# Optimization experiments

Measured on AMD Instinct MI355X. Metric: run time of the kernel, lower is better.

Reference implementation:

```python
import jax, jax.numpy as jnp
import numpy as np

ANCHOR_SIZES = [64.0, 128.0, 256.0]
ANCHOR_RATIOS = [0.5, 1.0, 2.0]
STD_SCALING = 1.0
RPN_STRIDE = 16
PRE_NMS_TOP_N = 3000
POST_NMS_TOP_N = 300
NMS_IOU_THRES = 0.7


def make_anchors():
    # ratios are sqrt'd as in the original __init__; anchors stored as (w, h)
    rs = [np.sqrt(r) for r in ANCHOR_RATIOS]
    a = [[s * r, s / r] for s in ANCHOR_SIZES for r in rs]
    return np.array(a, dtype=np.float32)  # [A, 2]


def setup_inputs() -> dict:
    key = jax.random.key(0)
    k1, k2 = jax.random.split(key)
    B, A, H, W = 4, 9, 34, 60
    rpn_scores = jax.random.uniform(k1, (B, A, H, W), dtype=jnp.float32)
    rpn_deltas = jax.random.normal(k2, (B, 4 * A, H, W), dtype=jnp.float32)
    input_image = jnp.zeros((B, 3, 544, 960), dtype=jnp.float32)  # only shape is used
    return {"rpn_scores": rpn_scores, "rpn_deltas": rpn_deltas, "input_image": input_image}


def _pairwise_iou(boxes):
    # boxes: [N, 4] in (x1, y1, x2, y2)
    x1, y1, x2, y2 = boxes[:, 0], boxes[:, 1], boxes[:, 2], boxes[:, 3]
    area = (x2 - x1) * (y2 - y1)
    iw = jnp.maximum(jnp.minimum(x2[:, None], x2[None, :]) - jnp.maximum(x1[:, None], x1[None, :]), 0.0)
    ih = jnp.maximum(jnp.minimum(y2[:, None], y2[None, :]) - jnp.maximum(y1[:, None], y1[None, :]), 0.0)
    inter = iw * ih
    union = area[:, None] + area[None, :] - inter
    return inter / jnp.maximum(union, 1e-8)


def _nms_single(boxes, probs):
    # pre-NMS top-N by score, then greedy IoU suppression, then post-NMS top-N (zero-padded)
    scores_k, idx = jax.lax.top_k(probs, PRE_NMS_TOP_N)
    boxes_k = boxes[idx]                                 # [pre_N, 4]
    iou = _pairwise_iou(boxes_k)                         # [pre_N, pre_N]

    def body(active, i):
        keep_i = active[i]
        sup = (iou[i] > NMS_IOU_THRES) & keep_i
        sup = sup.at[i].set(False)
        return active & ~sup, keep_i

    _, keep = jax.lax.scan(body, jnp.ones((PRE_NMS_TOP_N,), bool), jnp.arange(PRE_NMS_TOP_N))
    sel = jnp.where(keep, scores_k, -jnp.inf)
    _, kidx = jax.lax.top_k(sel, POST_NMS_TOP_N)
    valid = keep[kidx]
    return jnp.where(valid[:, None], boxes_k[kidx], 0.0)  # [post_N, 4]


def _forward(rpn_scores, rpn_deltas, input_image):
    B, A, H, W = rpn_scores.shape
    img_h = jnp.float32(input_image.shape[2])
    img_w = jnp.float32(input_image.shape[3])
    # NCHW -> NHWC -> [B,H,W,A,4]; channel layout is anchor-major, coord-minor
    deltas = (rpn_deltas * (1.0 / STD_SCALING)).transpose(0, 2, 3, 1).reshape(B, H, W, A, 4)
    ancs = jnp.asarray(make_anchors())                   # [A, 2] (w, h)
    aw, ah = ancs[:, 0], ancs[:, 1]
    # anchor centers on the RPN grid, at input-image scale
    cx = jnp.broadcast_to(((jnp.arange(W, dtype=jnp.float32) + 0.5) * RPN_STRIDE)[None, :, None], (H, W, A))
    cy = jnp.broadcast_to(((jnp.arange(H, dtype=jnp.float32) + 0.5) * RPN_STRIDE)[:, None, None], (H, W, A))
    tx, ty, tw, th = deltas[..., 0], deltas[..., 1], deltas[..., 2], deltas[..., 3]
    ctr_x = cx + tx * aw
    ctr_y = cy + ty * ah
    w1 = jnp.exp(tw) * aw
    h1 = jnp.exp(th) * ah
    x1 = ctr_x - 0.5 * w1
    y1 = ctr_y - 0.5 * h1
    x2 = x1 + w1
    y2 = y1 + h1
    x1 = jnp.clip(x1, 0.0, img_w - 1.0)
    x2 = jnp.clip(x2, 0.0, img_w - 1.0)
    y1 = jnp.clip(y1, 0.0, img_h - 1.0)
    y2 = jnp.clip(y2, 0.0, img_h - 1.0)
    boxes = jnp.stack([x1, y1, x2, y2], axis=-1)          # [B,H,W,A,4]
    boxes = boxes.transpose(0, 3, 1, 2, 4).reshape(B, -1, 4)  # [B, A*H*W, 4] (matches score layout)
    probs = rpn_scores.reshape(B, -1)
    return jax.vmap(_nms_single)(boxes, probs)            # [B, post_N, 4]


def reference(rpn_scores, rpn_deltas, input_image):
    return _forward(rpn_scores, rpn_deltas, input_image)
```

## Files before the change

### kernel.cpp

```cpp
#include <hip/hip_runtime.h>
#include <stdint.h>

typedef uint32_t u32;
typedef uint64_t u64;

#define NB 4
#define NA 9
#define NH 34
#define NW 60
#define HW (NH*NW)
#define NBOX (NA*HW)
#define PRE_NMS 3000
#define POST_NMS 300
#define NBUCKET 4096
#define SEGCAP 4096
#define NTH 1024
#define PER 18
#define NCAND 1088
#define MWc 17
#define NCHK 17

__device__ __constant__ float c_aw[9] = {
  45.254833995939045f, 64.0f,  90.50966799187808f,
  90.50966799187808f,  128.0f, 181.01933598375617f,
  181.01933598375617f, 256.0f, 362.03867196751233f };
__device__ __constant__ float c_ah[9] = {
  90.50966799187808f,  64.0f,  45.254833995939045f,
  181.01933598375617f, 128.0f, 90.50966799187808f,
  362.03867196751233f, 256.0f, 181.01933598375617f };

__device__ __forceinline__ u64 readlane64(u64 v, int lane) {
  u32 lo = __builtin_amdgcn_readlane((u32)(v & 0xffffffffull), lane);
  u32 hi = __builtin_amdgcn_readlane((u32)(v >> 32), lane);
  return ((u64)hi << 32) | lo;
}

__device__ __forceinline__ float4 decode_box(const float* __restrict__ dl, int idx) {
  int a = idx / HW;
  int r = idx - a * HW;
  int h = r / NW;
  int w = r - h * NW;
  const float* dp = dl + (4 * a) * HW + r;
  float tx = dp[0];
  float ty = dp[HW];
  float tw = dp[2 * HW];
  float th = dp[3 * HW];
  float aw = c_aw[a], ah = c_ah[a];
  float ctr_x = ((float)w + 0.5f) * 16.0f + tx * aw;
  float ctr_y = ((float)h + 0.5f) * 16.0f + ty * ah;
  float w1 = expf(tw) * aw;
  float h1 = expf(th) * ah;
  float x1 = ctr_x - 0.5f * w1;
  float y1 = ctr_y - 0.5f * h1;
  float x2 = x1 + w1;
  float y2 = y1 + h1;
  x1 = fminf(fmaxf(x1, 0.0f), 959.0f);
  x2 = fminf(fmaxf(x2, 0.0f), 959.0f);
  y1 = fminf(fmaxf(y1, 0.0f), 543.0f);
  y2 = fminf(fmaxf(y2, 0.0f), 543.0f);
  return make_float4(x1, y1, x2, y2);
}

__global__ void __launch_bounds__(NTH)
topk_rank_decode_kernel(const float* __restrict__ scores,
                        const float* __restrict__ deltas,
                        float4* __restrict__ boxes_ws)
{
  __shared__ u32 s_base[NBUCKET];
  __shared__ u32 s_cnt[NBUCKET];
  __shared__ u64 s_keys[SEGCAP];
  __shared__ u32 s_sfx[NTH];

  const int tid = threadIdx.x;
  const int b   = blockIdx.x;
  const float* sc = scores + b * NBOX;

  for (int t = tid; t < NBUCKET; t += NTH) s_cnt[t] = 0;
  __syncthreads();

  for (int m = 0; m < PER; ++m) {
    int i = tid + m * NTH;
    if (i < NBOX) {
      float s = sc[i];
      int bk = (int)(s * (float)NBUCKET);
      bk = bk < 0 ? 0 : (bk > NBUCKET - 1 ? NBUCKET - 1 : bk);
      atomicAdd(&s_cnt[bk], 1u);
    }
  }
  __syncthreads();

  u32 h0 = s_cnt[4*tid], h1 = s_cnt[4*tid+1], h2 = s_cnt[4*tid+2], h3 = s_cnt[4*tid+3];
  s_sfx[tid] = h0 + h1 + h2 + h3;
  __syncthreads();
  if (tid < 64) {
    const int l = tid;
    u32 v0,v1,v2,v3,v4,v5,v6,v7,v8,v9,v10,v11,v12,v13,v14,v15;
    {
      const u32* p = &s_sfx[l * 16];
      v0=p[0]; v1=p[1]; v2=p[2]; v3=p[3]; v4=p[4]; v5=p[5]; v6=p[6]; v7=p[7];
      v8=p[8]; v9=p[9]; v10=p[10]; v11=p[11]; v12=p[12]; v13=p[13]; v14=p[14]; v15=p[15];
    }
    v14+=v15; v13+=v14; v12+=v13; v11+=v12; v10+=v11; v9+=v10; v8+=v9; v7+=v8;
    v6+=v7; v5+=v6; v4+=v5; v3+=v4; v2+=v3; v1+=v2; v0+=v1;
    u32 tot = v0;
    u32 inc = tot;
    #pragma unroll
    for (int off = 1; off < 64; off <<= 1) {
      u32 x = (u32)__shfl_down((int)inc, off, 64);
      if (l + off < 64) inc += x;
    }
    u32 exc = inc - tot;
    {
      u32* p = &s_sfx[l * 16];
      p[0]=v0+exc; p[1]=v1+exc; p[2]=v2+exc; p[3]=v3+exc;
      p[4]=v4+exc; p[5]=v5+exc; p[6]=v6+exc; p[7]=v7+exc;
      p[8]=v8+exc; p[9]=v9+exc; p[10]=v10+exc; p[11]=v11+exc;
      p[12]=v12+exc; p[13]=v13+exc; p[14]=v14+exc; p[15]=v15+exc;
    }
  }
  __syncthreads();

  {
    u32 Gn = (tid < NTH - 1) ? s_sfx[tid + 1] : 0u;
    s_base[4*tid+3] = Gn;
    s_base[4*tid+2] = Gn + h3;
    s_base[4*tid+1] = Gn + h3 + h2;
    s_base[4*tid+0] = Gn + h3 + h2 + h1;
  }
  __syncthreads();

  for (int t = tid; t < NBUCKET; t += NTH) s_cnt[t] = 0;
  for (int t = tid; t < SEGCAP; t += NTH) s_keys[t] = 0ull;
  __syncthreads();

  for (int m = 0; m < PER; ++m) {
    int i = tid + m * NTH;
    if (i < NBOX) {
      float s = sc[i];
      int bk = (int)(s * (float)NBUCKET);
      bk = bk < 0 ? 0 : (bk > NBUCKET - 1 ? NBUCKET - 1 : bk);
      u32 base = s_base[bk];
      if (base < PRE_NMS) {
        u32 loc = atomicAdd(&s_cnt[bk], 1u);
        u32 pos = base + loc;
        if (pos < SEGCAP) {
          u64 key = ((u64)__float_as_uint(s) << 32) | (u32)(~(u32)i);
          s_keys[pos] = key;
        }
      }
    }
  }
  __syncthreads();

  const float* dl = deltas + b * (4 * NA * HW);
  for (int m = 0; m < SEGCAP / NTH; ++m) {
    int p = tid + m * NTH;
    u64 key = s_keys[p];
    float s = __uint_as_float((u32)(key >> 32));
    int bk = (int)(s * (float)NBUCKET);
    bk = bk < 0 ? 0 : (bk > NBUCKET - 1 ? NBUCKET - 1 : bk);
    u32 base = s_base[bk];
    u32 cnt  = s_cnt[bk];
    u32 local = 0;
    for (u32 q = base; q < base + cnt; ++q)
      local += (s_keys[q] > key) ? 1u : 0u;
    u32 R = base + local;
    if (key != 0ull && R < PRE_NMS) {
      int idx = (int)(~(u32)key);
      boxes_ws[b * PRE_NMS + R] = decode_box(dl, idx);
    }
  }
}

__global__ void __launch_bounds__(256)
mask_corner_kernel(const float4* __restrict__ boxes_ws, u64* __restrict__ masks2)
{
  const int wq = blockIdx.x;
  const int rb = blockIdx.y;
  const int b  = blockIdx.z;
  const int tid = threadIdx.x;
  __shared__ float4 s_cb[64];
  __shared__ float  s_ca[64];
  if (tid < 64) {
    int j = wq * 64 + tid;
    float4 v = boxes_ws[b * PRE_NMS + j];
    s_cb[tid] = v;
    s_ca[tid] = (v.z - v.x) * (v.w - v.y);
  }
  __syncthreads();
  int row = rb * 256 + tid;
  if (row < NCAND) {
    float4 r = boxes_ws[b * PRE_NMS + row];
    float ra = (r.z - r.x) * (r.w - r.y);
    u64 word = 0;
    #pragma unroll
    for (int k = 0; k < 64; ++k) {
      float4 cb = s_cb[k];
      float iw = fminf(r.z, cb.z) - fmaxf(r.x, cb.x);
      float ih = fminf(r.w, cb.w) - fmaxf(r.y, cb.y);
      iw = fmaxf(iw, 0.0f);
      ih = fmaxf(ih, 0.0f);
      float inter = iw * ih;
      float uni = ra + s_ca[k] - inter;
      word |= ((u64)(inter > 0.7f * fmaxf(uni, 1e-8f))) << k;
    }
    masks2[((size_t)b * NCAND + row) * MWc + wq] = word;
  }
}

__global__ void __launch_bounds__(128)
nms_reduce_kernel(const float4* __restrict__ boxes_ws,
                  const u64* __restrict__ masks2,
                  float* __restrict__ out)
{
  const int b = blockIdx.x;
  const int tid = threadIdx.x;
  const int wv = tid >> 6;
  const int lane = tid & 63;

  __shared__ __align__(16) u64 s_buf[2][64 * MWc];
  __shared__ u64 s_bm[MWc];
  __shared__ u32 s_kept[POST_NMS];
  __shared__ u32 s_nk;

  const u64* mbase = masks2 + (size_t)b * NCAND * MWc;

  if (wv == 1) {
    #pragma unroll
    for (int w = 0; w < MWc; ++w)
      s_buf[0][lane + w * 64] = mbase[lane + w * 64];
  } else if (lane < MWc) {
    s_bm[lane] = 0ull;
  }
  __syncthreads();

  int nk = 0;
  bool fin = false;

  for (int chunk = 0; chunk < NCHK; ++chunk) {
    if (wv == 1) {
      if (chunk + 1 < NCHK) {
        const u64* src = mbase + (size_t)(chunk + 1) * 64 * MWc;
        u64* dst = s_buf[(chunk + 1) & 1];
        #pragma unroll
        for (int w = 0; w < MWc; ++w)
          dst[lane + w * 64] = src[lane + w * 64];
      }
    } else if (!fin) {
      const u64* row = &s_buf[chunk & 1][lane * MWc];
      u64 s = 0ull;
      #pragma unroll
      for (int w = 0; w < MWc; ++w)
        s |= row[w] & s_bm[w];
      u64 D = row[chunk];
      u64 a = __ballot(s == 0ull);
      u64 supw = 0ull, keepm = 0ull;
      while (a) {
        int k = __ffsll((unsigned long long)a) - 1;
        a &= a - 1ull;
        if (!((supw >> k) & 1ull)) {
          keepm |= 1ull << k;
          if (lane == 0) s_kept[nk] = (u32)(chunk * 64 + k);
          ++nk;
          if (nk >= POST_NMS) { fin = true; break; }
          supw |= readlane64(D, k);
        }
      }
      if (lane == 0) s_bm[chunk] = keepm;
    }
    __syncthreads();
  }

  if (wv == 0) {
    if (nk < POST_NMS) {
      float4 kb[5];
      float  ka[5];
      #pragma unroll
      for (int s = 0; s < 5; ++s) {
        int t = s * 64 + lane;
        float4 v = make_float4(0.f, 0.f, 0.f, 0.f);
        if (t < nk) v = boxes_ws[b * PRE_NMS + s_kept[t]];
        kb[s] = v;
        ka[s] = (v.z - v.x) * (v.w - v.y);
      }
      for (int i = NCAND; i < PRE_NMS; ++i) {
        if (nk >= POST_NMS) break;
        float4 c = boxes_ws[b * PRE_NMS + i];
        float carea = (c.z - c.x) * (c.w - c.y);
        bool over = false;
        #pragma unroll
        for (int s = 0; s < 5; ++s) {
          if (s * 64 < nk) {
            if (s * 64 + lane < nk) {
              float iw = fminf(kb[s].z, c.z) - fmaxf(kb[s].x, c.x);
              float ih = fminf(kb[s].w, c.w) - fmaxf(kb[s].y, c.y);
              iw = fmaxf(iw, 0.0f);
              ih = fmaxf(ih, 0.0f);
              float inter = iw * ih;
              float uni = ka[s] + carea - inter;
              over = over || (inter > 0.7f * fmaxf(uni, 1e-8f));
            }
          }
        }
        if (__ballot((int)over) == 0ull) {
          int s = nk >> 6, l = nk & 63;
          #pragma unroll
          for (int q = 0; q < 5; ++q)
            if (q == s && lane == l) { kb[q] = c; ka[q] = carea; }
          if (lane == 0) s_kept[nk] = (u32)i;
          ++nk;
        }
      }
    }
    if (lane == 0) s_nk = (u32)nk;
  }
  __syncthreads();

  u32 fnk = s_nk;
  float4* outv = (float4*)out;
  for (int t = tid; t < POST_NMS; t += 128) {
    float4 v = make_float4(0.f, 0.f, 0.f, 0.f);
    if ((u32)t < fnk) v = boxes_ws[b * PRE_NMS + s_kept[t]];
    outv[b * POST_NMS + t] = v;
  }
}

__global__ void __launch_bounds__(NTH)
rpn_proposal_mono(const float* __restrict__ scores,
                  const float* __restrict__ deltas,
                  float* __restrict__ out)
{
  __shared__ __align__(16) char smem[16384 + 32768 + 4096];
  u32* s_hist = (u32*)smem;
  u64* s_cand = (u64*)(smem + 16384);
  u32* s_sfx  = (u32*)(smem + 16384 + 32768);
  float4* s_box = (float4*)smem;
  __shared__ u32 s_kept[POST_NMS];
  __shared__ u32 s_meta[4];

  const int tid = threadIdx.x;
  const int b   = blockIdx.x;
  const float* sc = scores + b * NBOX;

  for (int t = tid; t < NBUCKET; t += NTH) s_hist[t] = 0;
  if (tid < 4) s_meta[tid] = 0;
  __syncthreads();
  for (int m = 0; m < PER; ++m) {
    int i = tid + m * NTH;
    if (i < NBOX) {
      float s = sc[i];
      int bk = (int)(s * (float)NBUCKET);
      bk = bk < 0 ? 0 : (bk > NBUCKET - 1 ? NBUCKET - 1 : bk);
      atomicAdd(&s_hist[bk], 1u);
    }
  }
  __syncthreads();
  {
    u32 g = s_hist[4*tid] + s_hist[4*tid+1] + s_hist[4*tid+2] + s_hist[4*tid+3];
    s_sfx[tid] = g;
  }
  __syncthreads();
  for (int d = 1; d < NTH; d <<= 1) {
    u32 v = (tid + d < NTH) ? s_sfx[tid + d] : 0u;
    __syncthreads();
    s_sfx[tid] += v;
    __syncthreads();
  }
  {
    u32 sg  = s_sfx[tid];
    u32 sgn = (tid < NTH - 1) ? s_sfx[tid + 1] : 0u;
    if (sg >= PRE_NMS && sgn < PRE_NMS) {
      u32 c = sgn;
      for (int t = 4 * tid + 3; t >= 4 * tid; --t) {
        c += s_hist[t];
        if (c >= PRE_NMS) { s_meta[0] = (u32)t; s_meta[1] = c; break; }
      }
    }
  }
  __syncthreads();
  const u32 T = s_meta[0];
  for (int m = 0; m < PER; ++m) {
    int i = tid + m * NTH;
    if (i < NBOX) {
      float s = sc[i];
      int bk = (int)(s * (float)NBUCKET);
      bk = bk < 0 ? 0 : (bk > NBUCKET - 1 ? NBUCKET - 1 : bk);
      if ((u32)bk >= T) {
        u32 pos = atomicAdd(&s_meta[2], 1u);
        if (pos < SEGCAP) {
          u64 key = ((u64)__float_as_uint(s) << 32) | (u32)(~(u32)i);
          s_cand[pos] = key;
        }
      }
    }
  }
  __syncthreads();
  {
    u32 C = s_meta[2]; if (C > SEGCAP) C = SEGCAP;
    for (u32 p = C + tid; p < SEGCAP; p += NTH) s_cand[p] = 0ull;
  }
  for (int kk = 2; kk <= SEGCAP; kk <<= 1) {
    for (int j = kk >> 1; j > 0; j >>= 1) {
      __syncthreads();
      #pragma unroll
      for (int m = 0; m < 2; ++m) {
        int t = tid + m * NTH;
        int i = ((t & ~(j - 1)) << 1) | (t & (j - 1));
        int p = i | j;
        u64 a  = s_cand[i];
        u64 bb = s_cand[p];
        bool desc = (i & kk) == 0;
        bool sw = desc ? (a < bb) : (a > bb);
        if (sw) { s_cand[i] = bb; s_cand[p] = a; }
      }
    }
  }
  __syncthreads();
  const float* dl = deltas + b * (4 * NA * HW);
  float4 bx[3];
  #pragma unroll
  for (int m = 0; m < 3; ++m) {
    int k = tid + m * NTH;
    if (k < PRE_NMS) {
      u64 key = s_cand[k];
      bx[m] = decode_box(dl, (int)(~(u32)key));
    }
  }
  __syncthreads();
  #pragma unroll
  for (int m = 0; m < 3; ++m) {
    int k = tid + m * NTH;
    if (k < PRE_NMS) s_box[k] = bx[m];
  }
  __syncthreads();
  if (tid < 64) {
    const int lane = tid;
    float4 kb[5];
    float  ka[5];
    int nk = 0;
    for (int i = 0; i < PRE_NMS; ++i) {
      if (nk >= POST_NMS) break;
      float4 c = s_box[i];
      float carea = (c.z - c.x) * (c.w - c.y);
      bool over = false;
      #pragma unroll
      for (int s = 0; s < 5; ++s) {
        if (s * 64 < nk) {
          if (s * 64 + lane < nk) {
            float iw = fminf(kb[s].z, c.z) - fmaxf(kb[s].x, c.x);
            float ih = fminf(kb[s].w, c.w) - fmaxf(kb[s].y, c.y);
            iw = fmaxf(iw, 0.0f);
            ih = fmaxf(ih, 0.0f);
            float inter = iw * ih;
            float uni = ka[s] + carea - inter;
            over = over || (inter > 0.7f * fmaxf(uni, 1e-8f));
          }
        }
      }
      if (__ballot((int)over) == 0ull) {
        int s = nk >> 6, l = nk & 63;
        #pragma unroll
        for (int q = 0; q < 5; ++q)
          if (q == s && lane == l) { kb[q] = c; ka[q] = carea; }
        if (lane == 0) s_kept[nk] = (u32)i;
        ++nk;
      }
    }
    if (lane == 0) s_meta[3] = (u32)nk;
  }
  __syncthreads();
  if (tid < POST_NMS) {
    u32 nk = s_meta[3];
    float4 v = make_float4(0.0f, 0.0f, 0.0f, 0.0f);
    if ((u32)tid < nk) v = s_box[s_kept[tid]];
    ((float4*)out)[b * POST_NMS + tid] = v;
  }
}

extern "C" void kernel_launch(void* const* d_in, const int* in_sizes, int n_in,
                              void* d_out, int out_size, void* d_ws, size_t ws_size,
                              hipStream_t stream) {
  const float* scores = (const float*)d_in[0];
  const float* deltas = (const float*)d_in[1];
  (void)in_sizes; (void)n_in; (void)out_size;

  const size_t mask_off   = 196608;
  const size_t mask_bytes = (size_t)NB * NCAND * MWc * sizeof(u64);
  const size_t need       = mask_off + mask_bytes;

  if (ws_size >= need) {
    float4* boxes_ws = (float4*)d_ws;
    u64*    masks2   = (u64*)((char*)d_ws + mask_off);
    topk_rank_decode_kernel<<<dim3(NB), dim3(NTH), 0, stream>>>(scores, deltas, boxes_ws);
    mask_corner_kernel<<<dim3(MWc, (NCAND + 255) / 256, NB), dim3(256), 0, stream>>>(boxes_ws, masks2);
    nms_reduce_kernel<<<dim3(NB), dim3(128), 0, stream>>>(boxes_ws, masks2, (float*)d_out);
  } else {
    rpn_proposal_mono<<<dim3(NB), dim3(NTH), 0, stream>>>(scores, deltas, (float*)d_out);
  }
}
```

Measured before the change: 161.7 us.

## Transpose NMS mask layout, widen candidate window, and compute only needed triangle

The IoU bitmask grows from 1088 to 2048 precomputed candidates and is stored column-major (word-major), so each lane's loads in the reduce kernel are coalesced. Blocks whose columns are never needed for a given row range exit early, skipping roughly half of the mask computation. The reduce kernel drops its shared-memory double-buffer prefetch wave and runs as a single wave that reads the 32 mask words straight from global memory. Fewer candidates should now fall through to the slow serial fallback loop, but mask memory and the number of global loads per chunk both increase.

```diff
diff --git a/kernel.cpp b/kernel.cpp
--- a/kernel.cpp
+++ b/kernel.cpp
@@ -16,9 +16,8 @@
 #define SEGCAP 4096
 #define NTH 1024
 #define PER 18
-#define NCAND 1088
-#define MWc 17
-#define NCHK 17
+#define NCAND 2048
+#define MWT 32
 
 __device__ __constant__ float c_aw[9] = {
   45.254833995939045f, 64.0f,  90.50966799187808f,
@@ -173,11 +172,12 @@
 }
 
 __global__ void __launch_bounds__(256)
-mask_corner_kernel(const float4* __restrict__ boxes_ws, u64* __restrict__ masks2)
+mask_kernel_T(const float4* __restrict__ boxes_ws, u64* __restrict__ masksT)
 {
   const int wq = blockIdx.x;
   const int rb = blockIdx.y;
   const int b  = blockIdx.z;
+  if (wq > 4 * rb + 3) return;
   const int tid = threadIdx.x;
   __shared__ float4 s_cb[64];
   __shared__ float  s_ca[64];
@@ -188,139 +188,127 @@
     s_ca[tid] = (v.z - v.x) * (v.w - v.y);
   }
   __syncthreads();
-  int row = rb * 256 + tid;
-  if (row < NCAND) {
-    float4 r = boxes_ws[b * PRE_NMS + row];
-    float ra = (r.z - r.x) * (r.w - r.y);
-    u64 word = 0;
-    #pragma unroll
-    for (int k = 0; k < 64; ++k) {
-      float4 cb = s_cb[k];
-      float iw = fminf(r.z, cb.z) - fmaxf(r.x, cb.x);
-      float ih = fminf(r.w, cb.w) - fmaxf(r.y, cb.y);
-      iw = fmaxf(iw, 0.0f);
-      ih = fmaxf(ih, 0.0f);
-      float inter = iw * ih;
-      float uni = ra + s_ca[k] - inter;
-      word |= ((u64)(inter > 0.7f * fmaxf(uni, 1e-8f))) << k;
-    }
-    masks2[((size_t)b * NCAND + row) * MWc + wq] = word;
-  }
-}
-
-__global__ void __launch_bounds__(128)
+  int c = rb * 256 + tid;
+  float4 r = boxes_ws[b * PRE_NMS + c];
+  float ra = (r.z - r.x) * (r.w - r.y);
+  u64 word = 0;
+  #pragma unroll
+  for (int k = 0; k < 64; ++k) {
+    float4 cb = s_cb[k];
+    float iw = fminf(r.z, cb.z) - fmaxf(r.x, cb.x);
+    float ih = fminf(r.w, cb.w) - fmaxf(r.y, cb.y);
+    iw = fmaxf(iw, 0.0f);
+    ih = fmaxf(ih, 0.0f);
+    float inter = iw * ih;
+    float uni = ra + s_ca[k] - inter;
+    word |= ((u64)(inter > 0.7f * fmaxf(uni, 1e-8f))) << k;
+  }
+  masksT[((size_t)b * MWT + wq) * NCAND + c] = word;
+}
+
+__global__ void __launch_bounds__(64)
 nms_reduce_kernel(const float4* __restrict__ boxes_ws,
-                  const u64* __restrict__ masks2,
+                  const u64* __restrict__ masksT,
                   float* __restrict__ out)
 {
   const int b = blockIdx.x;
-  const int tid = threadIdx.x;
-  const int wv = tid >> 6;
-  const int lane = tid & 63;
-
-  __shared__ __align__(16) u64 s_buf[2][64 * MWc];
-  __shared__ u64 s_bm[MWc];
+  const int lane = threadIdx.x;
+  __shared__ u64 s_bm[MWT];
   __shared__ u32 s_kept[POST_NMS];
-  __shared__ u32 s_nk;
-
-  const u64* mbase = masks2 + (size_t)b * NCAND * MWc;
-
-  if (wv == 1) {
-    #pragma unroll
-    for (int w = 0; w < MWc; ++w)
-      s_buf[0][lane + w * 64] = mbase[lane + w * 64];
-  } else if (lane < MWc) {
-    s_bm[lane] = 0ull;
-  }
+
+  const u64* mtb = masksT + (size_t)b * MWT * NCAND;
+
+  if (lane < MWT) s_bm[lane] = 0ull;
   __syncthreads();
 
   int nk = 0;
   bool fin = false;
 
-  for (int chunk = 0; chunk < NCHK; ++chunk) {
-    if (wv == 1) {
-      if (chunk + 1 < NCHK) {
-        const u64* src = mbase + (size_t)(chunk + 1) * 64 * MWc;
-        u64* dst = s_buf[(chunk + 1) & 1];
-        #pragma unroll
-        for (int w = 0; w < MWc; ++w)
-          dst[lane + w * 64] = src[lane + w * 64];
-      }
-    } else if (!fin) {
-      const u64* row = &s_buf[chunk & 1][lane * MWc];
-      u64 s = 0ull;
-      #pragma unroll
-      for (int w = 0; w < MWc; ++w)
-        s |= row[w] & s_bm[w];
-      u64 D = row[chunk];
-      u64 a = __ballot(s == 0ull);
-      u64 supw = 0ull, keepm = 0ull;
-      while (a) {
-        int k = __ffsll((unsigned long long)a) - 1;
-        a &= a - 1ull;
-        if (!((supw >> k) & 1ull)) {
-          keepm |= 1ull << k;
-          if (lane == 0) s_kept[nk] = (u32)(chunk * 64 + k);
-          ++nk;
-          if (nk >= POST_NMS) { fin = true; break; }
-          supw |= readlane64(D, k);
-        }
-      }
-      if (lane == 0) s_bm[chunk] = keepm;
-    }
+  for (int j = 0; j < MWT && !fin; ++j) {
+    const int c = j * 64 + lane;
+    const u64* pc = mtb + c;
+    u64 v0  = pc[ 0*NCAND], v1  = pc[ 1*NCAND], v2  = pc[ 2*NCAND], v3  = pc[ 3*NCAND];
+    u64 v4  = pc[ 4*NCAND], v5  = pc[ 5*NCAND], v6  = pc[ 6*NCAND], v7  = pc[ 7*NCAND];
+    u64 v8  = pc[ 8*NCAND], v9  = pc[ 9*NCAND], v10 = pc[10*NCAND], v11 = pc[11*NCAND];
+    u64 v12 = pc[12*NCAND], v13 = pc[13*NCAND], v14 = pc[14*NCAND], v15 = pc[15*NCAND];
+    u64 v16 = pc[16*NCAND], v17 = pc[17*NCAND], v18 = pc[18*NCAND], v19 = pc[19*NCAND];
+    u64 v20 = pc[20*NCAND], v21 = pc[21*NCAND], v22 = pc[22*NCAND], v23 = pc[23*NCAND];
+    u64 v24 = pc[24*NCAND], v25 = pc[25*NCAND], v26 = pc[26*NCAND], v27 = pc[27*NCAND];
+    u64 v28 = pc[28*NCAND], v29 = pc[29*NCAND], v30 = pc[30*NCAND], v31 = pc[31*NCAND];
+    u64 D   = pc[(size_t)j * NCAND];
+
+    u64 s = (v0  & s_bm[0])  | (v1  & s_bm[1])  | (v2  & s_bm[2])  | (v3  & s_bm[3])
+          | (v4  & s_bm[4])  | (v5  & s_bm[5])  | (v6  & s_bm[6])  | (v7  & s_bm[7])
+          | (v8  & s_bm[8])  | (v9  & s_bm[9])  | (v10 & s_bm[10]) | (v11 & s_bm[11])
+          | (v12 & s_bm[12]) | (v13 & s_bm[13]) | (v14 & s_bm[14]) | (v15 & s_bm[15])
+          | (v16 & s_bm[16]) | (v17 & s_bm[17]) | (v18 & s_bm[18]) | (v19 & s_bm[19])
+          | (v20 & s_bm[20]) | (v21 & s_bm[21]) | (v22 & s_bm[22]) | (v23 & s_bm[23])
+          | (v24 & s_bm[24]) | (v25 & s_bm[25]) | (v26 & s_bm[26]) | (v27 & s_bm[27])
+          | (v28 & s_bm[28]) | (v29 & s_bm[29]) | (v30 & s_bm[30]) | (v31 & s_bm[31]);
+
+    u64 a = __ballot(s == 0ull);
+    u64 supw = 0ull, keepm = 0ull;
+    while (a) {
+      int k = __ffsll((unsigned long long)a) - 1;
+      a &= a - 1ull;
+      if (!((supw >> k) & 1ull)) {
+        keepm |= 1ull << k;
+        if (lane == 0) s_kept[nk] = (u32)(j * 64 + k);
+        ++nk;
+        if (nk >= POST_NMS) { fin = true; break; }
+        supw |= readlane64(D, k);
+      }
+    }
+    if (lane == 0) s_bm[j] = keepm;
     __syncthreads();
   }
 
-  if (wv == 0) {
-    if (nk < POST_NMS) {
-      float4 kb[5];
-      float  ka[5];
+  if (nk < POST_NMS) {
+    float4 kb[5];
+    float  ka[5];
+    #pragma unroll
+    for (int s = 0; s < 5; ++s) {
+      int t = s * 64 + lane;
+      float4 v = make_float4(0.f, 0.f, 0.f, 0.f);
+      if (t < nk) v = boxes_ws[b * PRE_NMS + s_kept[t]];
+      kb[s] = v;
+      ka[s] = (v.z - v.x) * (v.w - v.y);
+    }
+    for (int i = NCAND; i < PRE_NMS; ++i) {
+      if (nk >= POST_NMS) break;
+      float4 c = boxes_ws[b * PRE_NMS + i];
+      float carea = (c.z - c.x) * (c.w - c.y);
+      bool over = false;
       #pragma unroll
       for (int s = 0; s < 5; ++s) {
-        int t = s * 64 + lane;
-        float4 v = make_float4(0.f, 0.f, 0.f, 0.f);
-        if (t < nk) v = boxes_ws[b * PRE_NMS + s_kept[t]];
-        kb[s] = v;
-        ka[s] = (v.z - v.x) * (v.w - v.y);
-      }
-      for (int i = NCAND; i < PRE_NMS; ++i) {
-        if (nk >= POST_NMS) break;
-        float4 c = boxes_ws[b * PRE_NMS + i];
-        float carea = (c.z - c.x) * (c.w - c.y);
-        bool over = false;
-        #pragma unroll
-        for (int s = 0; s < 5; ++s) {
-          if (s * 64 < nk) {
-            if (s * 64 + lane < nk) {
-              float iw = fminf(kb[s].z, c.z) - fmaxf(kb[s].x, c.x);
-              float ih = fminf(kb[s].w, c.w) - fmaxf(kb[s].y, c.y);
-              iw = fmaxf(iw, 0.0f);
-              ih = fmaxf(ih, 0.0f);
-              float inter = iw * ih;
-              float uni = ka[s] + carea - inter;
-              over = over || (inter > 0.7f * fmaxf(uni, 1e-8f));
-            }
+        if (s * 64 < nk) {
+          if (s * 64 + lane < nk) {
+            float iw = fminf(kb[s].z, c.z) - fmaxf(kb[s].x, c.x);
+            float ih = fminf(kb[s].w, c.w) - fmaxf(kb[s].y, c.y);
+            iw = fmaxf(iw, 0.0f);
+            ih = fmaxf(ih, 0.0f);
+            float inter = iw * ih;
+            float uni = ka[s] + carea - inter;
+            over = over || (inter > 0.7f * fmaxf(uni, 1e-8f));
           }
         }
-        if (__ballot((int)over) == 0ull) {
-          int s = nk >> 6, l = nk & 63;
-          #pragma unroll
-          for (int q = 0; q < 5; ++q)
-            if (q == s && lane == l) { kb[q] = c; ka[q] = carea; }
-          if (lane == 0) s_kept[nk] = (u32)i;
-          ++nk;
-        }
-      }
-    }
-    if (lane == 0) s_nk = (u32)nk;
-  }
-  __syncthreads();
-
-  u32 fnk = s_nk;
+      }
+      if (__ballot((int)over) == 0ull) {
+        int s = nk >> 6, l = nk & 63;
+        #pragma unroll
+        for (int q = 0; q < 5; ++q)
+          if (q == s && lane == l) { kb[q] = c; ka[q] = carea; }
+        if (lane == 0) s_kept[nk] = (u32)i;
+        ++nk;
+      }
+    }
+  }
+  __syncthreads();
+
   float4* outv = (float4*)out;
-  for (int t = tid; t < POST_NMS; t += 128) {
+  for (int t = lane; t < POST_NMS; t += 64) {
     float4 v = make_float4(0.f, 0.f, 0.f, 0.f);
-    if ((u32)t < fnk) v = boxes_ws[b * PRE_NMS + s_kept[t]];
+    if (t < nk) v = boxes_ws[b * PRE_NMS + s_kept[t]];
     outv[b * POST_NMS + t] = v;
   }
 }
@@ -485,15 +473,15 @@
   (void)in_sizes; (void)n_in; (void)out_size;
 
   const size_t mask_off   = 196608;
-  const size_t mask_bytes = (size_t)NB * NCAND * MWc * sizeof(u64);
+  const size_t mask_bytes = (size_t)NB * MWT * NCAND * sizeof(u64);
   const size_t need       = mask_off + mask_bytes;
 
   if (ws_size >= need) {
     float4* boxes_ws = (float4*)d_ws;
-    u64*    masks2   = (u64*)((char*)d_ws + mask_off);
+    u64*    masksT   = (u64*)((char*)d_ws + mask_off);
     topk_rank_decode_kernel<<<dim3(NB), dim3(NTH), 0, stream>>>(scores, deltas, boxes_ws);
-    mask_corner_kernel<<<dim3(MWc, (NCAND + 255) / 256, NB), dim3(256), 0, stream>>>(boxes_ws, masks2);
-    nms_reduce_kernel<<<dim3(NB), dim3(128), 0, stream>>>(boxes_ws, masks2, (float*)d_out);
+    mask_kernel_T<<<dim3(MWT, NCAND / 256, NB), dim3(256), 0, stream>>>(boxes_ws, masksT);
+    nms_reduce_kernel<<<dim3(NB), dim3(64), 0, stream>>>(boxes_ws, masksT, (float*)d_out);
   } else {
     rpn_proposal_mono<<<dim3(NB), dim3(NTH), 0, stream>>>(scores, deltas, (float*)d_out);
   }
```

Result: faster. 146.0 us (-9.7%).
